# Kernel tuning notes

Hardware: AMD Instinct MI355X
Metric: run time of the kernel (lower is better)

The kernel has to match this reference:

```python
import jax, jax.numpy as jnp
import numpy as np

VOCAB, EMBED, HIDDEN = 50000, 256, 512
BATCH, SEQ = 64, 512


def setup_inputs() -> dict:
    key = jax.random.key(0)
    ks = jax.random.split(key, 20)
    s = 0.05  # small init scale to keep gates out of saturation
    inp = {
        "tokens": jax.random.randint(ks[0], (BATCH, SEQ), 0, VOCAB, dtype=jnp.int64),
        "emb": jax.random.normal(ks[1], (VOCAB, EMBED), jnp.float32) * s,
        "W1f": jax.random.normal(ks[2], (EMBED, 4 * HIDDEN), jnp.float32) * s,
        "U1f": jax.random.normal(ks[3], (HIDDEN, 4 * HIDDEN), jnp.float32) * s,
        "b1f": jax.random.normal(ks[4], (4 * HIDDEN,), jnp.float32) * s,
        "W2f": jax.random.normal(ks[5], (HIDDEN, 4 * HIDDEN), jnp.float32) * s,
        "U2f": jax.random.normal(ks[6], (HIDDEN, 4 * HIDDEN), jnp.float32) * s,
        "b2f": jax.random.normal(ks[7], (4 * HIDDEN,), jnp.float32) * s,
        "W1b": jax.random.normal(ks[8], (EMBED, 4 * HIDDEN), jnp.float32) * s,
        "U1b": jax.random.normal(ks[9], (HIDDEN, 4 * HIDDEN), jnp.float32) * s,
        "b1b": jax.random.normal(ks[10], (4 * HIDDEN,), jnp.float32) * s,
        "W2b": jax.random.normal(ks[11], (HIDDEN, 4 * HIDDEN), jnp.float32) * s,
        "U2b": jax.random.normal(ks[12], (HIDDEN, 4 * HIDDEN), jnp.float32) * s,
        "b2b": jax.random.normal(ks[13], (4 * HIDDEN,), jnp.float32) * s,
        "Wd": jax.random.normal(ks[14], (2 * HIDDEN, 5), jnp.float32) * s,
        "bd": jax.random.normal(ks[15], (5,), jnp.float32) * s,
    }
    return inp


def _lstm_cell(x, h, c, W, U, b):
    # Keras gate order: i, f, g (candidate), o
    z = x @ W + h @ U + b
    i, f, g, o = jnp.split(z, 4, axis=-1)
    c = jax.nn.sigmoid(f) * c + jax.nn.sigmoid(i) * jnp.tanh(g)
    h = jax.nn.sigmoid(o) * jnp.tanh(c)
    return h, c


def _run_stack(xs, W1, U1, b1, W2, U2, b2):
    # xs: [T, B, E]; stacked 2-layer LSTM, return last hidden of layer 2: [B, H]
    B = xs.shape[1]
    H = U1.shape[0]
    init = tuple(jnp.zeros((B, H), xs.dtype) for _ in range(4))

    def step(carry, x_t):
        h1, c1, h2, c2 = carry
        h1, c1 = _lstm_cell(x_t, h1, c1, W1, U1, b1)
        h2, c2 = _lstm_cell(h1, h2, c2, W2, U2, b2)
        return (h1, c1, h2, c2), None

    (h1, c1, h2, c2), _ = jax.lax.scan(step, init, xs)
    return h2


def reference(tokens, emb, W1f, U1f, b1f, W2f, U2f, b2f,
              W1b, U1b, b1b, W2b, U2b, b2b, Wd, bd):
    x = emb[tokens]                 # [B, T, E]
    xs = jnp.swapaxes(x, 0, 1)      # [T, B, E]
    h_fwd = _run_stack(xs, W1f, U1f, b1f, W2f, U2f, b2f)          # [B, H]
    h_bwd = _run_stack(xs[::-1], W1b, U1b, b1b, W2b, U2b, b2b)    # [B, H]
    feat = jnp.concatenate([h_fwd, h_bwd], axis=-1)               # [B, 2H]
    return feat @ Wd + bd                                         # [B, 5]
```

## Files before the change

### kernel.cpp

```cpp
#include <hip/hip_runtime.h>
#include <hip/hip_bf16.h>

#define TSEQ 512
#define NB   64
#define NE   256
#define NH   512
#define NG   2048

static const size_t OFF_W1  = 0;
static const size_t OFF_W2  = 6291456;
static const size_t OFF_X   = 14680064;
static const size_t OFF_H1  = 31457280;
static const size_t OFF_H2  = 31981568;
static const size_t OFF_HF  = 32505856;
static const size_t OFF_CNT = 32636928;

typedef __bf16 v8bf __attribute__((ext_vector_type(8)));
typedef float  v4f  __attribute__((ext_vector_type(4)));

#define MFMA16(a_, b_, c_) __builtin_amdgcn_mfma_f32_16x16x32_bf16((a_), (b_), (c_), 0, 0, 0)

static __device__ __forceinline__ v8bf load_h8(const __bf16* p) {
    unsigned long long lo = __hip_atomic_load((unsigned long long*)p,     __ATOMIC_RELAXED, __HIP_MEMORY_SCOPE_AGENT);
    unsigned long long hi = __hip_atomic_load((unsigned long long*)p + 1, __ATOMIC_RELAXED, __HIP_MEMORY_SCOPE_AGENT);
    union { unsigned long long q[2]; v8bf v; } u;
    u.q[0] = lo; u.q[1] = hi;
    return u.v;
}

static __device__ __forceinline__ unsigned short bf16_bits(float f) {
    __bf16 b = (__bf16)f;
    return __builtin_bit_cast(unsigned short, b);
}

__global__ void wconv_kernel(const float* __restrict__ Wf, const float* __restrict__ Uf,
                             const float* __restrict__ Wb, const float* __restrict__ Ub,
                             char* __restrict__ dst, int NC, int KX)
{
    int id = blockIdx.x * 256 + threadIdx.x;
    int j    = id & 7;
    int lane = (id >> 3) & 63;
    int t    = (id >> 9) & 1;
    int rest = id >> 10;
    int c    = rest % NC;
    int ds   = rest / NC;
    int slice = ds & 63;
    int dirr  = ds >> 6;
    int coll = t * 16 + (lane & 15);
    int k    = c * 32 + (lane >> 4) * 8 + j;
    int gate = coll >> 3, jjj = coll & 7;
    int zcol = gate * 512 + slice * 8 + jjj;
    const float* W = dirr ? Wb : Wf;
    const float* U = dirr ? Ub : Uf;
    float v = (k < KX) ? W[(size_t)k * NG + zcol] : U[(size_t)(k - KX) * NG + zcol];
    ((__bf16*)dst)[id] = (__bf16)v;
}

__global__ void gather_x_kernel(const int* __restrict__ tokens, const float* __restrict__ emb,
                                char* __restrict__ ws)
{
    size_t id = (size_t)blockIdx.x * 256 + threadIdx.x;
    int j  = (int)(id & 7);
    int m  = (int)((id >> 3) & 63);
    int kb = (int)((id >> 9) & 31);
    int t  = (int)(id >> 14);
    int tok = tokens[m * TSEQ + t];
    float v = emb[(size_t)tok * NE + kb * 8 + j];
    ((__bf16*)(ws + OFF_X))[(size_t)t * 16384 + (kb * 64 + m) * 8 + j] = (__bf16)v;
    if (id < 16384) ((int*)(ws + OFF_CNT))[id] = 0;
}

template<int LAYER>
__device__ void run_layer(char* __restrict__ ws, const char* __restrict__ smem,
                          int dir, int slice, int tid,
                          const float* __restrict__ bb)
{
    const int lane = tid & 63;
    const int wv   = tid >> 6;
    const int colc = lane & 15;
    const int q    = lane >> 4;
    const int m0   = wv * 16;
    const int jj   = colc & 7;
    const int hcol = slice * 8 + jj;

    __bf16* h1ring = (__bf16*)(ws + OFF_H1 + (size_t)dir * (4 * 65536));
    __bf16* h2ring = (__bf16*)(ws + OFF_H2 + (size_t)dir * (4 * 65536));
    const char* Xfrag = ws + OFF_X;
    __bf16* hfin = (__bf16*)(ws + OFF_HF) + (size_t)dir * (NB * NH);

    int* T = (int*)(ws + OFF_CNT);
    const int rep = ((slice << 2) | wv) & 15;
    int* p1   = T + (dir * 2 + 0) * 4096 + rep * 256 + wv * 64 + lane;
    int* p2   = T + (dir * 2 + 1) * 4096 + rep * 256 + wv * 64 + lane;
    int* ownb = T + (dir * 2 + LAYER) * 4096;

    const float bi  = bb[hcol];
    const float bf_ = bb[512 + hcol];
    const float bg  = bb[1024 + hcol];
    const float bo  = bb[1536 + hcol];

    float cst[4] = {0.f, 0.f, 0.f, 0.f};

    const int aoff = (m0 + colc) * 8;

    #pragma unroll 1
    for (int s = 0; s < TSEQ; ++s) {
        v4f acc0a = {0,0,0,0}, acc1a = {0,0,0,0};
        v4f acc0b = {0,0,0,0}, acc1b = {0,0,0,0};

        if (LAYER == 0) {
            const int xs = dir ? (TSEQ - 1 - s) : s;
            const char* xb = Xfrag + (size_t)xs * 32768;
            #pragma unroll
            for (int c = 0; c < 8; ++c) {
                v8bf a  = *(const v8bf*)(xb + (((4 * c + q) * 64 + m0 + colc) * 16));
                v8bf w0 = *(const v8bf*)(smem + (c * 2 + 0) * 1024 + lane * 16);
                v8bf w1 = *(const v8bf*)(smem + (c * 2 + 1) * 1024 + lane * 16);
                if (c & 1) { acc0b = MFMA16(a, w0, acc0b); acc1b = MFMA16(a, w1, acc1b); }
                else       { acc0a = MFMA16(a, w0, acc0a); acc1a = MFMA16(a, w1, acc1a); }
            }
        }

        {
            const int t1 = LAYER ? s + 1 : s;
            const int t2 = LAYER ? s : s - 3;
            if (t1 > 0) {
                while (true) {
                    int v1 = __hip_atomic_load(p1, __ATOMIC_RELAXED, __HIP_MEMORY_SCOPE_AGENT);
                    bool ok = (v1 >= t1);
                    if (t2 > 0) {
                        int v2 = __hip_atomic_load(p2, __ATOMIC_RELAXED, __HIP_MEMORY_SCOPE_AGENT);
                        ok = ok && (v2 >= t2);
                    }
                    if (__all(ok)) break;
                }
            }
        }

        if (LAYER == 0) {
            if (s > 0) {
                const __bf16* hb = h1ring + (size_t)((s - 1) & 3) * 32768;
                v8bf ah[16];
                #pragma unroll
                for (int c = 0; c < 16; ++c)
                    ah[c] = load_h8(hb + (4 * c + q) * 512 + aoff);
                __builtin_amdgcn_sched_barrier(0);
                #pragma unroll
                for (int c = 0; c < 16; ++c) {
                    v8bf w0 = *(const v8bf*)(smem + ((8 + c) * 2 + 0) * 1024 + lane * 16);
                    v8bf w1 = *(const v8bf*)(smem + ((8 + c) * 2 + 1) * 1024 + lane * 16);
                    if (c & 1) { acc0b = MFMA16(ah[c], w0, acc0b); acc1b = MFMA16(ah[c], w1, acc1b); }
                    else       { acc0a = MFMA16(ah[c], w0, acc0a); acc1a = MFMA16(ah[c], w1, acc1a); }
                }
            }
        } else {
            const __bf16* hb1 = h1ring + (size_t)(s & 3) * 32768;
            v8bf a0[16], a1[16];
            #pragma unroll
            for (int c = 0; c < 16; ++c)
                a0[c] = load_h8(hb1 + (4 * c + q) * 512 + aoff);
            if (s > 0) {
                const __bf16* hb2 = h2ring + (size_t)((s - 1) & 3) * 32768;
                #pragma unroll
                for (int c = 0; c < 16; ++c)
                    a1[c] = load_h8(hb2 + (4 * c + q) * 512 + aoff);
            }
            __builtin_amdgcn_sched_barrier(0);
            #pragma unroll
            for (int c = 0; c < 16; ++c) {
                v8bf w0 = *(const v8bf*)(smem + (c * 2 + 0) * 1024 + lane * 16);
                v8bf w1 = *(const v8bf*)(smem + (c * 2 + 1) * 1024 + lane * 16);
                if (c & 1) { acc0b = MFMA16(a0[c], w0, acc0b); acc1b = MFMA16(a0[c], w1, acc1b); }
                else       { acc0a = MFMA16(a0[c], w0, acc0a); acc1a = MFMA16(a0[c], w1, acc1a); }
            }
            if (s > 0) {
                #pragma unroll
                for (int c = 0; c < 16; ++c) {
                    v8bf w0 = *(const v8bf*)(smem + ((16 + c) * 2 + 0) * 1024 + lane * 16);
                    v8bf w1 = *(const v8bf*)(smem + ((16 + c) * 2 + 1) * 1024 + lane * 16);
                    if (c & 1) { acc0b = MFMA16(a1[c], w0, acc0b); acc1b = MFMA16(a1[c], w1, acc1b); }
                    else       { acc0a = MFMA16(a1[c], w0, acc0a); acc1a = MFMA16(a1[c], w1, acc1a); }
                }
            }
        }

        v4f z0 = acc0a + acc0b;
        v4f z1 = acc1a + acc1b;

        float hv[4];
        #pragma unroll
        for (int r = 0; r < 4; ++r) {
            float p0 = __shfl_xor(z0[r], 8, 64);
            float p1 = __shfl_xor(z1[r], 8, 64);
            float zi, zf, zg, zo;
            if (colc < 8) { zi = z0[r]; zf = p0;    zg = z1[r]; zo = p1;    }
            else          { zi = p0;    zf = z0[r]; zg = p1;    zo = z1[r]; }
            zi += bi; zf += bf_; zg += bg; zo += bo;
            float gi = 1.f / (1.f + __expf(-zi));
            float gf = 1.f / (1.f + __expf(-zf));
            float gg = 1.f - 2.f / (1.f + __expf(2.f * zg));
            float go = 1.f / (1.f + __expf(-zo));
            float cn = gf * cst[r] + gi * gg;
            cst[r] = cn;
            float th = 1.f - 2.f / (1.f + __expf(2.f * cn));
            hv[r] = go * th;
        }

        __bf16* hd = (LAYER ? h2ring : h1ring) + (size_t)(s & 3) * 32768;
        #pragma unroll
        for (int r = 0; r < 4; ++r) {
            float pv = __shfl_xor(hv[r], 1, 64);
            int m = m0 + q * 4 + r;
            if (((colc & 1) == 0) && (colc < 8)) {
                unsigned val = (unsigned)bf16_bits(hv[r]) | ((unsigned)bf16_bits(pv) << 16);
                __hip_atomic_store((unsigned*)(hd + (slice * 64 + m) * 8 + colc), val,
                                   __ATOMIC_RELAXED, __HIP_MEMORY_SCOPE_AGENT);
            }
            if (LAYER == 1 && s == TSEQ - 1 && colc < 8)
                hfin[(size_t)m * NH + hcol] = (__bf16)hv[r];
        }

        asm volatile("s_waitcnt vmcnt(0)" ::: "memory");
        if (lane < 16)
            __hip_atomic_store(ownb + lane * 256 + wv * 64 + slice, s + 1,
                               __ATOMIC_RELAXED, __HIP_MEMORY_SCOPE_AGENT);
    }
}

__global__ __launch_bounds__(256, 1) void lstm_persist(
    char* __restrict__ ws,
    const float* __restrict__ b1f, const float* __restrict__ b2f,
    const float* __restrict__ b1b, const float* __restrict__ b2b)
{
    const int tid   = threadIdx.x;
    const int bid   = blockIdx.x;
    const int dir   = bid >> 7;
    const int layer = (bid >> 6) & 1;
    const int slice = bid & 63;

    const int NC = layer ? 32 : 24;
    const int wbytes = NC * 2048;

    __shared__ char smem[65536];
    {
        const char* wsrc = ws + (layer ? OFF_W2 : OFF_W1)
                         + (size_t)(dir * 64 + slice) * (size_t)wbytes;
        for (int i = tid * 16; i < wbytes; i += 256 * 16)
            *(uint4*)(smem + i) = *(const uint4*)(wsrc + i);
    }
    __syncthreads();

    const float* bb = layer ? (dir ? b2b : b2f) : (dir ? b1b : b1f);
    if (layer == 0) run_layer<0>(ws, smem, dir, slice, tid, bb);
    else            run_layer<1>(ws, smem, dir, slice, tid, bb);
}

__global__ void head_kernel(const char* __restrict__ ws, const float* __restrict__ Wd,
                            const float* __restrict__ bd, float* __restrict__ out)
{
    int b = blockIdx.x;
    int lane = threadIdx.x;
    const __bf16* hfF = (const __bf16*)(ws + OFF_HF) + (size_t)b * NH;
    const __bf16* hfB = (const __bf16*)(ws + OFF_HF) + (size_t)(NB * NH) + (size_t)b * NH;
    #pragma unroll
    for (int o = 0; o < 5; ++o) {
        float sum = 0.f;
        for (int k = lane; k < 2 * NH; k += 64) {
            float fv = (k < NH) ? (float)hfF[k] : (float)hfB[k - NH];
            sum += fv * Wd[(size_t)k * 5 + o];
        }
        #pragma unroll
        for (int off = 32; off > 0; off >>= 1) sum += __shfl_down(sum, off, 64);
        if (lane == 0) out[b * 5 + o] = sum + bd[o];
    }
}

extern "C" void kernel_launch(void* const* d_in, const int* in_sizes, int n_in,
                              void* d_out, int out_size, void* d_ws, size_t ws_size,
                              hipStream_t stream)
{
    const int*   tokens = (const int*)  d_in[0];
    const float* emb    = (const float*)d_in[1];
    const float* W1f    = (const float*)d_in[2];
    const float* U1f    = (const float*)d_in[3];
    const float* b1f    = (const float*)d_in[4];
    const float* W2f    = (const float*)d_in[5];
    const float* U2f    = (const float*)d_in[6];
    const float* b2f    = (const float*)d_in[7];
    const float* W1b    = (const float*)d_in[8];
    const float* U1b    = (const float*)d_in[9];
    const float* b1b    = (const float*)d_in[10];
    const float* W2b    = (const float*)d_in[11];
    const float* U2b    = (const float*)d_in[12];
    const float* b2b    = (const float*)d_in[13];
    const float* Wd     = (const float*)d_in[14];
    const float* bd     = (const float*)d_in[15];
    char* ws = (char*)d_ws;

    wconv_kernel<<<12288, 256, 0, stream>>>(W1f, U1f, W1b, U1b, ws + OFF_W1, 24, 256);
    wconv_kernel<<<16384, 256, 0, stream>>>(W2f, U2f, W2b, U2b, ws + OFF_W2, 32, 512);
    gather_x_kernel<<<32768, 256, 0, stream>>>(tokens, emb, ws);
    lstm_persist<<<256, 256, 0, stream>>>(ws, b1f, b2f, b1b, b2b);
    head_kernel<<<NB, 64, 0, stream>>>(ws, Wd, bd, (float*)d_out);
}
```

Before: 3.545 ms.

## Validate hidden-state fragments with XOR shadow copies instead of draining stores

Each hidden-state write now also writes an XOR-masked shadow copy, with the mask alternating per ring pass. Readers reload until data and shadow agree, so the s_waitcnt vmcnt(0) before publishing the step counter can be removed. The ring shrinks from 4 to 3 slots, and layer 1 now waits on its two dependencies separately so it can start the h1 matmul before h2 is ready. The cost is doubled store and load traffic, possible retry loops, and reliance on relaxed-ordering assumptions for correctness.

```diff
diff --git a/kernel.cpp b/kernel.cpp
--- a/kernel.cpp
+++ b/kernel.cpp
@@ -11,9 +11,13 @@
 static const size_t OFF_W2  = 6291456;
 static const size_t OFF_X   = 14680064;
 static const size_t OFF_H1  = 31457280;
-static const size_t OFF_H2  = 31981568;
-static const size_t OFF_HF  = 32505856;
-static const size_t OFF_CNT = 32636928;
+static const size_t OFF_H2  = 31850496;
+static const size_t OFF_S1  = 32243712;
+static const size_t OFF_S2  = 32636928;
+static const size_t OFF_HF  = 33030144;
+static const size_t OFF_CNT = 33161216;
+
+#define SHDELTA 393216
 
 typedef __bf16 v8bf __attribute__((ext_vector_type(8)));
 typedef float  v4f  __attribute__((ext_vector_type(4)));
@@ -32,6 +36,34 @@
     __bf16 b = (__bf16)f;
     return __builtin_bit_cast(unsigned short, b);
 }
+
+static __device__ __forceinline__ unsigned frag_ok(v8bf d, v8bf sh, unsigned m) {
+    union { v8bf v; unsigned u[4]; } a, b;
+    a.v = d; b.v = sh;
+    unsigned x = (a.u[0] ^ b.u[0] ^ m) | (a.u[1] ^ b.u[1] ^ m)
+               | (a.u[2] ^ b.u[2] ^ m) | (a.u[3] ^ b.u[3] ^ m);
+    return (unsigned)(x == 0u);
+}
+
+#define LOAD_VALIDATE16(dst_, base_, mm_)                                      \
+    {                                                                          \
+        const __bf16* _b  = (base_);                                           \
+        const __bf16* _sb = _b + SHDELTA;                                      \
+        const unsigned _m = (mm_);                                             \
+        while (true) {                                                         \
+            v8bf _sh[16];                                                      \
+            _Pragma("unroll")                                                  \
+            for (int c = 0; c < 16; ++c) {                                     \
+                dst_[c] = load_h8(_b  + (4 * c + q) * 512 + aoff);             \
+                _sh[c]  = load_h8(_sb + (4 * c + q) * 512 + aoff);             \
+            }                                                                  \
+            __builtin_amdgcn_sched_barrier(0);                                 \
+            unsigned _ok = 1u;                                                 \
+            _Pragma("unroll")                                                  \
+            for (int c = 0; c < 16; ++c) _ok &= frag_ok(dst_[c], _sh[c], _m);  \
+            if (__all((int)_ok)) break;                                        \
+        }                                                                      \
+    }
 
 __global__ void wconv_kernel(const float* __restrict__ Wf, const float* __restrict__ Uf,
                              const float* __restrict__ Wb, const float* __restrict__ Ub,
@@ -67,6 +99,9 @@
     int tok = tokens[m * TSEQ + t];
     float v = emb[(size_t)tok * NE + kb * 8 + j];
     ((__bf16*)(ws + OFF_X))[(size_t)t * 16384 + (kb * 64 + m) * 8 + j] = (__bf16)v;
+    if (id < 393216) {
+        ((unsigned*)(ws + OFF_H1))[id] = (id < 196608) ? 0u : 0x3F803F80u;
+    }
     if (id < 16384) ((int*)(ws + OFF_CNT))[id] = 0;
 }
 
@@ -83,8 +118,8 @@
     const int jj   = colc & 7;
     const int hcol = slice * 8 + jj;
 
-    __bf16* h1ring = (__bf16*)(ws + OFF_H1 + (size_t)dir * (4 * 65536));
-    __bf16* h2ring = (__bf16*)(ws + OFF_H2 + (size_t)dir * (4 * 65536));
+    __bf16* h1ring = (__bf16*)(ws + OFF_H1 + (size_t)dir * (3 * 65536));
+    __bf16* h2ring = (__bf16*)(ws + OFF_H2 + (size_t)dir * (3 * 65536));
     const char* Xfrag = ws + OFF_X;
     __bf16* hfin = (__bf16*)(ws + OFF_HF) + (size_t)dir * (NB * NH);
 
@@ -103,48 +138,44 @@
 
     const int aoff = (m0 + colc) * 8;
 
+    int cs = 0, ps = 0, cp = 0, pp = 0;
+
     #pragma unroll 1
     for (int s = 0; s < TSEQ; ++s) {
         v4f acc0a = {0,0,0,0}, acc1a = {0,0,0,0};
         v4f acc0b = {0,0,0,0}, acc1b = {0,0,0,0};
 
         if (LAYER == 0) {
-            const int xs = dir ? (TSEQ - 1 - s) : s;
-            const char* xb = Xfrag + (size_t)xs * 32768;
-            #pragma unroll
-            for (int c = 0; c < 8; ++c) {
-                v8bf a  = *(const v8bf*)(xb + (((4 * c + q) * 64 + m0 + colc) * 16));
-                v8bf w0 = *(const v8bf*)(smem + (c * 2 + 0) * 1024 + lane * 16);
-                v8bf w1 = *(const v8bf*)(smem + (c * 2 + 1) * 1024 + lane * 16);
-                if (c & 1) { acc0b = MFMA16(a, w0, acc0b); acc1b = MFMA16(a, w1, acc1b); }
-                else       { acc0a = MFMA16(a, w0, acc0a); acc1a = MFMA16(a, w1, acc1a); }
-            }
-        }
-
-        {
-            const int t1 = LAYER ? s + 1 : s;
-            const int t2 = LAYER ? s : s - 3;
-            if (t1 > 0) {
-                while (true) {
-                    int v1 = __hip_atomic_load(p1, __ATOMIC_RELAXED, __HIP_MEMORY_SCOPE_AGENT);
-                    bool ok = (v1 >= t1);
-                    if (t2 > 0) {
-                        int v2 = __hip_atomic_load(p2, __ATOMIC_RELAXED, __HIP_MEMORY_SCOPE_AGENT);
-                        ok = ok && (v2 >= t2);
+            {
+                const int xs = dir ? (TSEQ - 1 - s) : s;
+                const char* xb = Xfrag + (size_t)xs * 32768;
+                #pragma unroll
+                for (int c = 0; c < 8; ++c) {
+                    v8bf a  = *(const v8bf*)(xb + (((4 * c + q) * 64 + m0 + colc) * 16));
+                    v8bf w0 = *(const v8bf*)(smem + (c * 2 + 0) * 1024 + lane * 16);
+                    v8bf w1 = *(const v8bf*)(smem + (c * 2 + 1) * 1024 + lane * 16);
+                    if (c & 1) { acc0b = MFMA16(a, w0, acc0b); acc1b = MFMA16(a, w1, acc1b); }
+                    else       { acc0a = MFMA16(a, w0, acc0a); acc1a = MFMA16(a, w1, acc1a); }
+                }
+            }
+            {
+                const int t1 = s;
+                const int t2 = s - 2;
+                if (t1 > 0) {
+                    while (true) {
+                        int v1 = __hip_atomic_load(p1, __ATOMIC_RELAXED, __HIP_MEMORY_SCOPE_AGENT);
+                        bool ok = (v1 >= t1);
+                        if (t2 > 0) {
+                            int v2 = __hip_atomic_load(p2, __ATOMIC_RELAXED, __HIP_MEMORY_SCOPE_AGENT);
+                            ok = ok && (v2 >= t2);
+                        }
+                        if (__all(ok)) break;
                     }
-                    if (__all(ok)) break;
-                }
-            }
-        }
-
-        if (LAYER == 0) {
+                }
+            }
             if (s > 0) {
-                const __bf16* hb = h1ring + (size_t)((s - 1) & 3) * 32768;
                 v8bf ah[16];
-                #pragma unroll
-                for (int c = 0; c < 16; ++c)
-                    ah[c] = load_h8(hb + (4 * c + q) * 512 + aoff);
-                __builtin_amdgcn_sched_barrier(0);
+                LOAD_VALIDATE16(ah, h1ring + (size_t)ps * 32768, pp ? 0x40004000u : 0u);
                 #pragma unroll
                 for (int c = 0; c < 16; ++c) {
                     v8bf w0 = *(const v8bf*)(smem + ((8 + c) * 2 + 0) * 1024 + lane * 16);
@@ -154,26 +185,31 @@
                 }
             }
         } else {
-            const __bf16* hb1 = h1ring + (size_t)(s & 3) * 32768;
-            v8bf a0[16], a1[16];
-            #pragma unroll
-            for (int c = 0; c < 16; ++c)
-                a0[c] = load_h8(hb1 + (4 * c + q) * 512 + aoff);
+            {
+                const int t1 = s + 1;
+                while (true) {
+                    int v1 = __hip_atomic_load(p1, __ATOMIC_RELAXED, __HIP_MEMORY_SCOPE_AGENT);
+                    if (__all(v1 >= t1)) break;
+                }
+            }
+            {
+                v8bf a0[16];
+                LOAD_VALIDATE16(a0, h1ring + (size_t)cs * 32768, cp ? 0x40004000u : 0u);
+                #pragma unroll
+                for (int c = 0; c < 16; ++c) {
+                    v8bf w0 = *(const v8bf*)(smem + (c * 2 + 0) * 1024 + lane * 16);
+                    v8bf w1 = *(const v8bf*)(smem + (c * 2 + 1) * 1024 + lane * 16);
+                    if (c & 1) { acc0b = MFMA16(a0[c], w0, acc0b); acc1b = MFMA16(a0[c], w1, acc1b); }
+                    else       { acc0a = MFMA16(a0[c], w0, acc0a); acc1a = MFMA16(a0[c], w1, acc1a); }
+                }
+            }
             if (s > 0) {
-                const __bf16* hb2 = h2ring + (size_t)((s - 1) & 3) * 32768;
-                #pragma unroll
-                for (int c = 0; c < 16; ++c)
-                    a1[c] = load_h8(hb2 + (4 * c + q) * 512 + aoff);
-            }
-            __builtin_amdgcn_sched_barrier(0);
-            #pragma unroll
-            for (int c = 0; c < 16; ++c) {
-                v8bf w0 = *(const v8bf*)(smem + (c * 2 + 0) * 1024 + lane * 16);
-                v8bf w1 = *(const v8bf*)(smem + (c * 2 + 1) * 1024 + lane * 16);
-                if (c & 1) { acc0b = MFMA16(a0[c], w0, acc0b); acc1b = MFMA16(a0[c], w1, acc1b); }
-                else       { acc0a = MFMA16(a0[c], w0, acc0a); acc1a = MFMA16(a0[c], w1, acc1a); }
-            }
-            if (s > 0) {
+                while (true) {
+                    int v2 = __hip_atomic_load(p2, __ATOMIC_RELAXED, __HIP_MEMORY_SCOPE_AGENT);
+                    if (__all(v2 >= s)) break;
+                }
+                v8bf a1[16];
+                LOAD_VALIDATE16(a1, h2ring + (size_t)ps * 32768, pp ? 0x40004000u : 0u);
                 #pragma unroll
                 for (int c = 0; c < 16; ++c) {
                     v8bf w0 = *(const v8bf*)(smem + ((16 + c) * 2 + 0) * 1024 + lane * 16);
@@ -191,10 +227,10 @@
         #pragma unroll
         for (int r = 0; r < 4; ++r) {
             float p0 = __shfl_xor(z0[r], 8, 64);
-            float p1 = __shfl_xor(z1[r], 8, 64);
+            float p1v = __shfl_xor(z1[r], 8, 64);
             float zi, zf, zg, zo;
-            if (colc < 8) { zi = z0[r]; zf = p0;    zg = z1[r]; zo = p1;    }
-            else          { zi = p0;    zf = z0[r]; zg = p1;    zo = z1[r]; }
+            if (colc < 8) { zi = z0[r]; zf = p0;    zg = z1[r]; zo = p1v;   }
+            else          { zi = p0;    zf = z0[r]; zg = p1v;   zo = z1[r]; }
             zi += bi; zf += bf_; zg += bg; zo += bo;
             float gi = 1.f / (1.f + __expf(-zi));
             float gf = 1.f / (1.f + __expf(-zf));
@@ -206,7 +242,8 @@
             hv[r] = go * th;
         }
 
-        __bf16* hd = (LAYER ? h2ring : h1ring) + (size_t)(s & 3) * 32768;
+        __bf16* hd = (LAYER ? h2ring : h1ring) + (size_t)cs * 32768;
+        const unsigned mw = cp ? 0x40004000u : 0u;
         #pragma unroll
         for (int r = 0; r < 4; ++r) {
             float pv = __shfl_xor(hv[r], 1, 64);
@@ -215,15 +252,21 @@
                 unsigned val = (unsigned)bf16_bits(hv[r]) | ((unsigned)bf16_bits(pv) << 16);
                 __hip_atomic_store((unsigned*)(hd + (slice * 64 + m) * 8 + colc), val,
                                    __ATOMIC_RELAXED, __HIP_MEMORY_SCOPE_AGENT);
+                __hip_atomic_store((unsigned*)(hd + SHDELTA + (slice * 64 + m) * 8 + colc), val ^ mw,
+                                   __ATOMIC_RELAXED, __HIP_MEMORY_SCOPE_AGENT);
             }
             if (LAYER == 1 && s == TSEQ - 1 && colc < 8)
                 hfin[(size_t)m * NH + hcol] = (__bf16)hv[r];
         }
 
-        asm volatile("s_waitcnt vmcnt(0)" ::: "memory");
+        __builtin_amdgcn_sched_barrier(0);
         if (lane < 16)
             __hip_atomic_store(ownb + lane * 256 + wv * 64 + slice, s + 1,
                                __ATOMIC_RELAXED, __HIP_MEMORY_SCOPE_AGENT);
+
+        ps = cs; pp = cp;
+        cs = (cs == 2) ? 0 : cs + 1;
+        if (cs == 0) cp ^= 1;
     }
 }
 
```

Result: slower. 4.779 ms (+34.8%).

## Embed parity tag bits in hidden-state payload to validate ring reads without store fence

Applied to the files above, without the earlier changes.

Hidden values are clamped to below 1 so bit 14 of each bf16 is free, and that bit now carries a per-ring-lap parity tag. Readers check the tag on every loaded fragment and spin until all fragments match, then clear the bit. This lets writers drop the s_waitcnt vmcnt(0) before publishing their step counter. The risk is that counters can become visible before the data, which the tag check is meant to catch, and the clamp slightly changes numerics.

```diff
diff --git a/kernel.cpp b/kernel.cpp
--- a/kernel.cpp
+++ b/kernel.cpp
@@ -32,6 +32,53 @@
     __bf16 b = (__bf16)f;
     return __builtin_bit_cast(unsigned short, b);
 }
+
+static __device__ __forceinline__ unsigned frag_chk_clr(v8bf* f, unsigned pm) {
+    union { v8bf v; unsigned u[4]; } a; a.v = *f;
+    unsigned bad = ((a.u[0] ^ pm) | (a.u[1] ^ pm) | (a.u[2] ^ pm) | (a.u[3] ^ pm)) & 0x40004000u;
+    a.u[0] &= 0xBFFFBFFFu; a.u[1] &= 0xBFFFBFFFu;
+    a.u[2] &= 0xBFFFBFFFu; a.u[3] &= 0xBFFFBFFFu;
+    *f = a.v;
+    return bad;
+}
+
+#define LOAD_VALIDATE16(dst_, base_, pm_)                                      \
+    {                                                                          \
+        const __bf16* _b  = (base_);                                           \
+        const unsigned _pm = (pm_);                                            \
+        while (true) {                                                         \
+            _Pragma("unroll")                                                  \
+            for (int c = 0; c < 16; ++c)                                       \
+                dst_[c] = load_h8(_b + (4 * c + q) * 512 + aoff);              \
+            __builtin_amdgcn_sched_barrier(0);                                 \
+            unsigned _bad = 0u;                                                \
+            _Pragma("unroll")                                                  \
+            for (int c = 0; c < 16; ++c) _bad |= frag_chk_clr(&dst_[c], _pm);  \
+            if (__all(_bad == 0u)) break;                                      \
+        }                                                                      \
+    }
+
+#define LOAD_VALIDATE32(d0_, b0_, pm0_, d1_, b1_, pm1_)                        \
+    {                                                                          \
+        const __bf16* _b0 = (b0_);                                             \
+        const __bf16* _b1 = (b1_);                                             \
+        const unsigned _p0 = (pm0_), _p1 = (pm1_);                             \
+        while (true) {                                                         \
+            _Pragma("unroll")                                                  \
+            for (int c = 0; c < 16; ++c)                                       \
+                d0_[c] = load_h8(_b0 + (4 * c + q) * 512 + aoff);              \
+            _Pragma("unroll")                                                  \
+            for (int c = 0; c < 16; ++c)                                       \
+                d1_[c] = load_h8(_b1 + (4 * c + q) * 512 + aoff);              \
+            __builtin_amdgcn_sched_barrier(0);                                 \
+            unsigned _bad = 0u;                                                \
+            _Pragma("unroll")                                                  \
+            for (int c = 0; c < 16; ++c) _bad |= frag_chk_clr(&d0_[c], _p0);   \
+            _Pragma("unroll")                                                  \
+            for (int c = 0; c < 16; ++c) _bad |= frag_chk_clr(&d1_[c], _p1);   \
+            if (__all(_bad == 0u)) break;                                      \
+        }                                                                      \
+    }
 
 __global__ void wconv_kernel(const float* __restrict__ Wf, const float* __restrict__ Uf,
                              const float* __restrict__ Wb, const float* __restrict__ Ub,
@@ -67,7 +114,8 @@
     int tok = tokens[m * TSEQ + t];
     float v = emb[(size_t)tok * NE + kb * 8 + j];
     ((__bf16*)(ws + OFF_X))[(size_t)t * 16384 + (kb * 64 + m) * 8 + j] = (__bf16)v;
-    if (id < 16384) ((int*)(ws + OFF_CNT))[id] = 0;
+    if (id < 262144) ((unsigned*)(ws + OFF_H1))[id] = 0x40004000u;
+    if (id < 16384)  ((int*)(ws + OFF_CNT))[id] = 0;
 }
 
 template<int LAYER>
@@ -107,6 +155,9 @@
     for (int s = 0; s < TSEQ; ++s) {
         v4f acc0a = {0,0,0,0}, acc1a = {0,0,0,0};
         v4f acc0b = {0,0,0,0}, acc1b = {0,0,0,0};
+
+        const unsigned pmW  = ((s >> 2) & 1)       ? 0x40004000u : 0u;
+        const unsigned pmRp = (((s - 1) >> 2) & 1) ? 0x40004000u : 0u;
 
         if (LAYER == 0) {
             const int xs = dir ? (TSEQ - 1 - s) : s;
@@ -139,12 +190,8 @@
 
         if (LAYER == 0) {
             if (s > 0) {
-                const __bf16* hb = h1ring + (size_t)((s - 1) & 3) * 32768;
                 v8bf ah[16];
-                #pragma unroll
-                for (int c = 0; c < 16; ++c)
-                    ah[c] = load_h8(hb + (4 * c + q) * 512 + aoff);
-                __builtin_amdgcn_sched_barrier(0);
+                LOAD_VALIDATE16(ah, h1ring + (size_t)((s - 1) & 3) * 32768, pmRp);
                 #pragma unroll
                 for (int c = 0; c < 16; ++c) {
                     v8bf w0 = *(const v8bf*)(smem + ((8 + c) * 2 + 0) * 1024 + lane * 16);
@@ -154,18 +201,14 @@
                 }
             }
         } else {
-            const __bf16* hb1 = h1ring + (size_t)(s & 3) * 32768;
+            const unsigned pmRc = pmW;
             v8bf a0[16], a1[16];
-            #pragma unroll
-            for (int c = 0; c < 16; ++c)
-                a0[c] = load_h8(hb1 + (4 * c + q) * 512 + aoff);
             if (s > 0) {
-                const __bf16* hb2 = h2ring + (size_t)((s - 1) & 3) * 32768;
-                #pragma unroll
-                for (int c = 0; c < 16; ++c)
-                    a1[c] = load_h8(hb2 + (4 * c + q) * 512 + aoff);
-            }
-            __builtin_amdgcn_sched_barrier(0);
+                LOAD_VALIDATE32(a0, h1ring + (size_t)(s & 3) * 32768, pmRc,
+                                a1, h2ring + (size_t)((s - 1) & 3) * 32768, pmRp);
+            } else {
+                LOAD_VALIDATE16(a0, h1ring + (size_t)(s & 3) * 32768, pmRc);
+            }
             #pragma unroll
             for (int c = 0; c < 16; ++c) {
                 v8bf w0 = *(const v8bf*)(smem + (c * 2 + 0) * 1024 + lane * 16);
@@ -191,10 +234,10 @@
         #pragma unroll
         for (int r = 0; r < 4; ++r) {
             float p0 = __shfl_xor(z0[r], 8, 64);
-            float p1 = __shfl_xor(z1[r], 8, 64);
+            float p1v = __shfl_xor(z1[r], 8, 64);
             float zi, zf, zg, zo;
-            if (colc < 8) { zi = z0[r]; zf = p0;    zg = z1[r]; zo = p1;    }
-            else          { zi = p0;    zf = z0[r]; zg = p1;    zo = z1[r]; }
+            if (colc < 8) { zi = z0[r]; zf = p0;    zg = z1[r]; zo = p1v;   }
+            else          { zi = p0;    zf = z0[r]; zg = p1v;   zo = z1[r]; }
             zi += bi; zf += bf_; zg += bg; zo += bo;
             float gi = 1.f / (1.f + __expf(-zi));
             float gf = 1.f / (1.f + __expf(-zf));
@@ -203,7 +246,7 @@
             float cn = gf * cst[r] + gi * gg;
             cst[r] = cn;
             float th = 1.f - 2.f / (1.f + __expf(2.f * cn));
-            hv[r] = go * th;
+            hv[r] = fminf(fmaxf(go * th, -0.99609375f), 0.99609375f);
         }
 
         __bf16* hd = (LAYER ? h2ring : h1ring) + (size_t)(s & 3) * 32768;
@@ -212,7 +255,7 @@
             float pv = __shfl_xor(hv[r], 1, 64);
             int m = m0 + q * 4 + r;
             if (((colc & 1) == 0) && (colc < 8)) {
-                unsigned val = (unsigned)bf16_bits(hv[r]) | ((unsigned)bf16_bits(pv) << 16);
+                unsigned val = ((unsigned)bf16_bits(hv[r]) | ((unsigned)bf16_bits(pv) << 16)) | pmW;
                 __hip_atomic_store((unsigned*)(hd + (slice * 64 + m) * 8 + colc), val,
                                    __ATOMIC_RELAXED, __HIP_MEMORY_SCOPE_AGENT);
             }
@@ -220,7 +263,7 @@
                 hfin[(size_t)m * NH + hcol] = (__bf16)hv[r];
         }
 
-        asm volatile("s_waitcnt vmcnt(0)" ::: "memory");
+        __builtin_amdgcn_sched_barrier(0);
         if (lane < 16)
             __hip_atomic_store(ownb + lane * 256 + wv * 64 + slice, s + 1,
                                __ATOMIC_RELAXED, __HIP_MEMORY_SCOPE_AGENT);
```

New measurement: 3.675 ms. 1.04x slower.

## Halve persistent LSTM grid so each block owns two hidden slices

Applied to the files above, without the earlier changes.

The persistent LSTM kernel now launches 128 blocks instead of 256, and each block processes two adjacent 8-column hidden slices. It loads both weight tiles into up to 128 KB of dynamic shared memory and reuses each activation fragment across twice as many MFMAs. It also adds a short s_sleep in the spin-wait loop to reduce polling pressure. The aim is fewer participants in the per-step cross-block synchronization and better reuse of the loaded h fragments. The cost is twice the serial MFMA and gate work per block on the critical recurrent path, and the sleep can add wake-up latency.

```diff
diff --git a/kernel.cpp b/kernel.cpp
--- a/kernel.cpp
+++ b/kernel.cpp
@@ -72,7 +72,7 @@
 
 template<int LAYER>
 __device__ void run_layer(char* __restrict__ ws, const char* __restrict__ smem,
-                          int dir, int slice, int tid,
+                          int dir, int jp, int tid,
                           const float* __restrict__ bb)
 {
     const int lane = tid & 63;
@@ -81,7 +81,9 @@
     const int q    = lane >> 4;
     const int m0   = wv * 16;
     const int jj   = colc & 7;
-    const int hcol = slice * 8 + jj;
+    const int sA   = jp * 2;
+    const int sB   = sA + 1;
+    const int WB   = LAYER ? 65536 : 49152;
 
     __bf16* h1ring = (__bf16*)(ws + OFF_H1 + (size_t)dir * (4 * 65536));
     __bf16* h2ring = (__bf16*)(ws + OFF_H2 + (size_t)dir * (4 * 65536));
@@ -89,35 +91,49 @@
     __bf16* hfin = (__bf16*)(ws + OFF_HF) + (size_t)dir * (NB * NH);
 
     int* T = (int*)(ws + OFF_CNT);
-    const int rep = ((slice << 2) | wv) & 15;
+    const int rep = ((sA << 2) | wv) & 15;
     int* p1   = T + (dir * 2 + 0) * 4096 + rep * 256 + wv * 64 + lane;
     int* p2   = T + (dir * 2 + 1) * 4096 + rep * 256 + wv * 64 + lane;
     int* ownb = T + (dir * 2 + LAYER) * 4096;
 
-    const float bi  = bb[hcol];
-    const float bf_ = bb[512 + hcol];
-    const float bg  = bb[1024 + hcol];
-    const float bo  = bb[1536 + hcol];
-
-    float cst[4] = {0.f, 0.f, 0.f, 0.f};
+    float bi[2], bf_[2], bg_[2], bo_[2];
+    #pragma unroll
+    for (int g = 0; g < 2; ++g) {
+        const int hc = (sA + g) * 8 + jj;
+        bi[g]  = bb[hc];
+        bf_[g] = bb[512 + hc];
+        bg_[g] = bb[1024 + hc];
+        bo_[g] = bb[1536 + hc];
+    }
+
+    float cst[2][4] = {{0.f,0.f,0.f,0.f},{0.f,0.f,0.f,0.f}};
 
     const int aoff = (m0 + colc) * 8;
 
     #pragma unroll 1
     for (int s = 0; s < TSEQ; ++s) {
-        v4f acc0a = {0,0,0,0}, acc1a = {0,0,0,0};
-        v4f acc0b = {0,0,0,0}, acc1b = {0,0,0,0};
+        v4f az[2][2][2];
+        #pragma unroll
+        for (int g = 0; g < 2; ++g)
+            #pragma unroll
+            for (int p = 0; p < 2; ++p)
+                #pragma unroll
+                for (int ab = 0; ab < 2; ++ab)
+                    az[g][p][ab] = (v4f){0.f, 0.f, 0.f, 0.f};
 
         if (LAYER == 0) {
             const int xs = dir ? (TSEQ - 1 - s) : s;
             const char* xb = Xfrag + (size_t)xs * 32768;
             #pragma unroll
             for (int c = 0; c < 8; ++c) {
-                v8bf a  = *(const v8bf*)(xb + (((4 * c + q) * 64 + m0 + colc) * 16));
-                v8bf w0 = *(const v8bf*)(smem + (c * 2 + 0) * 1024 + lane * 16);
-                v8bf w1 = *(const v8bf*)(smem + (c * 2 + 1) * 1024 + lane * 16);
-                if (c & 1) { acc0b = MFMA16(a, w0, acc0b); acc1b = MFMA16(a, w1, acc1b); }
-                else       { acc0a = MFMA16(a, w0, acc0a); acc1a = MFMA16(a, w1, acc1a); }
+                v8bf a = *(const v8bf*)(xb + (((4 * c + q) * 64 + m0 + colc) * 16));
+                #pragma unroll
+                for (int g = 0; g < 2; ++g) {
+                    v8bf w0 = *(const v8bf*)(smem + g * WB + (c * 2 + 0) * 1024 + lane * 16);
+                    v8bf w1 = *(const v8bf*)(smem + g * WB + (c * 2 + 1) * 1024 + lane * 16);
+                    az[g][0][c & 1] = MFMA16(a, w0, az[g][0][c & 1]);
+                    az[g][1][c & 1] = MFMA16(a, w1, az[g][1][c & 1]);
+                }
             }
         }
 
@@ -133,6 +149,7 @@
                         ok = ok && (v2 >= t2);
                     }
                     if (__all(ok)) break;
+                    __builtin_amdgcn_s_sleep(4);
                 }
             }
         }
@@ -147,10 +164,13 @@
                 __builtin_amdgcn_sched_barrier(0);
                 #pragma unroll
                 for (int c = 0; c < 16; ++c) {
-                    v8bf w0 = *(const v8bf*)(smem + ((8 + c) * 2 + 0) * 1024 + lane * 16);
-                    v8bf w1 = *(const v8bf*)(smem + ((8 + c) * 2 + 1) * 1024 + lane * 16);
-                    if (c & 1) { acc0b = MFMA16(ah[c], w0, acc0b); acc1b = MFMA16(ah[c], w1, acc1b); }
-                    else       { acc0a = MFMA16(ah[c], w0, acc0a); acc1a = MFMA16(ah[c], w1, acc1a); }
+                    #pragma unroll
+                    for (int g = 0; g < 2; ++g) {
+                        v8bf w0 = *(const v8bf*)(smem + g * WB + ((8 + c) * 2 + 0) * 1024 + lane * 16);
+                        v8bf w1 = *(const v8bf*)(smem + g * WB + ((8 + c) * 2 + 1) * 1024 + lane * 16);
+                        az[g][0][c & 1] = MFMA16(ah[c], w0, az[g][0][c & 1]);
+                        az[g][1][c & 1] = MFMA16(ah[c], w1, az[g][1][c & 1]);
+                    }
                 }
             }
         } else {
@@ -168,62 +188,77 @@
             __builtin_amdgcn_sched_barrier(0);
             #pragma unroll
             for (int c = 0; c < 16; ++c) {
-                v8bf w0 = *(const v8bf*)(smem + (c * 2 + 0) * 1024 + lane * 16);
-                v8bf w1 = *(const v8bf*)(smem + (c * 2 + 1) * 1024 + lane * 16);
-                if (c & 1) { acc0b = MFMA16(a0[c], w0, acc0b); acc1b = MFMA16(a0[c], w1, acc1b); }
-                else       { acc0a = MFMA16(a0[c], w0, acc0a); acc1a = MFMA16(a0[c], w1, acc1a); }
+                #pragma unroll
+                for (int g = 0; g < 2; ++g) {
+                    v8bf w0 = *(const v8bf*)(smem + g * WB + (c * 2 + 0) * 1024 + lane * 16);
+                    v8bf w1 = *(const v8bf*)(smem + g * WB + (c * 2 + 1) * 1024 + lane * 16);
+                    az[g][0][c & 1] = MFMA16(a0[c], w0, az[g][0][c & 1]);
+                    az[g][1][c & 1] = MFMA16(a0[c], w1, az[g][1][c & 1]);
+                }
             }
             if (s > 0) {
                 #pragma unroll
                 for (int c = 0; c < 16; ++c) {
-                    v8bf w0 = *(const v8bf*)(smem + ((16 + c) * 2 + 0) * 1024 + lane * 16);
-                    v8bf w1 = *(const v8bf*)(smem + ((16 + c) * 2 + 1) * 1024 + lane * 16);
-                    if (c & 1) { acc0b = MFMA16(a1[c], w0, acc0b); acc1b = MFMA16(a1[c], w1, acc1b); }
-                    else       { acc0a = MFMA16(a1[c], w0, acc0a); acc1a = MFMA16(a1[c], w1, acc1a); }
-                }
-            }
-        }
-
-        v4f z0 = acc0a + acc0b;
-        v4f z1 = acc1a + acc1b;
-
-        float hv[4];
+                    #pragma unroll
+                    for (int g = 0; g < 2; ++g) {
+                        v8bf w0 = *(const v8bf*)(smem + g * WB + ((16 + c) * 2 + 0) * 1024 + lane * 16);
+                        v8bf w1 = *(const v8bf*)(smem + g * WB + ((16 + c) * 2 + 1) * 1024 + lane * 16);
+                        az[g][0][c & 1] = MFMA16(a1[c], w0, az[g][0][c & 1]);
+                        az[g][1][c & 1] = MFMA16(a1[c], w1, az[g][1][c & 1]);
+                    }
+                }
+            }
+        }
+
+        float hv[2][4];
         #pragma unroll
-        for (int r = 0; r < 4; ++r) {
-            float p0 = __shfl_xor(z0[r], 8, 64);
-            float p1 = __shfl_xor(z1[r], 8, 64);
-            float zi, zf, zg, zo;
-            if (colc < 8) { zi = z0[r]; zf = p0;    zg = z1[r]; zo = p1;    }
-            else          { zi = p0;    zf = z0[r]; zg = p1;    zo = z1[r]; }
-            zi += bi; zf += bf_; zg += bg; zo += bo;
-            float gi = 1.f / (1.f + __expf(-zi));
-            float gf = 1.f / (1.f + __expf(-zf));
-            float gg = 1.f - 2.f / (1.f + __expf(2.f * zg));
-            float go = 1.f / (1.f + __expf(-zo));
-            float cn = gf * cst[r] + gi * gg;
-            cst[r] = cn;
-            float th = 1.f - 2.f / (1.f + __expf(2.f * cn));
-            hv[r] = go * th;
+        for (int g = 0; g < 2; ++g) {
+            v4f z0 = az[g][0][0] + az[g][0][1];
+            v4f z1 = az[g][1][0] + az[g][1][1];
+            #pragma unroll
+            for (int r = 0; r < 4; ++r) {
+                float p0 = __shfl_xor(z0[r], 8, 64);
+                float p1v = __shfl_xor(z1[r], 8, 64);
+                float zi, zf, zg, zo;
+                if (colc < 8) { zi = z0[r]; zf = p0;    zg = z1[r]; zo = p1v;   }
+                else          { zi = p0;    zf = z0[r]; zg = p1v;   zo = z1[r]; }
+                zi += bi[g]; zf += bf_[g]; zg += bg_[g]; zo += bo_[g];
+                float gi = 1.f / (1.f + __expf(-zi));
+                float gf = 1.f / (1.f + __expf(-zf));
+                float gg = 1.f - 2.f / (1.f + __expf(2.f * zg));
+                float go = 1.f / (1.f + __expf(-zo));
+                float cn = gf * cst[g][r] + gi * gg;
+                cst[g][r] = cn;
+                float th = 1.f - 2.f / (1.f + __expf(2.f * cn));
+                hv[g][r] = go * th;
+            }
         }
 
         __bf16* hd = (LAYER ? h2ring : h1ring) + (size_t)(s & 3) * 32768;
         #pragma unroll
-        for (int r = 0; r < 4; ++r) {
-            float pv = __shfl_xor(hv[r], 1, 64);
-            int m = m0 + q * 4 + r;
-            if (((colc & 1) == 0) && (colc < 8)) {
-                unsigned val = (unsigned)bf16_bits(hv[r]) | ((unsigned)bf16_bits(pv) << 16);
-                __hip_atomic_store((unsigned*)(hd + (slice * 64 + m) * 8 + colc), val,
-                                   __ATOMIC_RELAXED, __HIP_MEMORY_SCOPE_AGENT);
-            }
-            if (LAYER == 1 && s == TSEQ - 1 && colc < 8)
-                hfin[(size_t)m * NH + hcol] = (__bf16)hv[r];
+        for (int g = 0; g < 2; ++g) {
+            const int sl = sA + g;
+            #pragma unroll
+            for (int r = 0; r < 4; ++r) {
+                float pv = __shfl_xor(hv[g][r], 1, 64);
+                int m = m0 + q * 4 + r;
+                if (((colc & 1) == 0) && (colc < 8)) {
+                    unsigned val = (unsigned)bf16_bits(hv[g][r]) | ((unsigned)bf16_bits(pv) << 16);
+                    __hip_atomic_store((unsigned*)(hd + (sl * 64 + m) * 8 + colc), val,
+                                       __ATOMIC_RELAXED, __HIP_MEMORY_SCOPE_AGENT);
+                }
+                if (LAYER == 1 && s == TSEQ - 1 && colc < 8)
+                    hfin[(size_t)m * NH + sl * 8 + jj] = (__bf16)hv[g][r];
+            }
         }
 
         asm volatile("s_waitcnt vmcnt(0)" ::: "memory");
-        if (lane < 16)
-            __hip_atomic_store(ownb + lane * 256 + wv * 64 + slice, s + 1,
+        if (lane < 16) {
+            __hip_atomic_store(ownb + lane * 256 + wv * 64 + sA, s + 1,
                                __ATOMIC_RELAXED, __HIP_MEMORY_SCOPE_AGENT);
+            __hip_atomic_store(ownb + lane * 256 + wv * 64 + sB, s + 1,
+                               __ATOMIC_RELAXED, __HIP_MEMORY_SCOPE_AGENT);
+        }
     }
 }
 
@@ -232,27 +267,26 @@
     const float* __restrict__ b1f, const float* __restrict__ b2f,
     const float* __restrict__ b1b, const float* __restrict__ b2b)
 {
+    extern __shared__ char smem[];
     const int tid   = threadIdx.x;
     const int bid   = blockIdx.x;
-    const int dir   = bid >> 7;
-    const int layer = (bid >> 6) & 1;
-    const int slice = bid & 63;
-
-    const int NC = layer ? 32 : 24;
-    const int wbytes = NC * 2048;
-
-    __shared__ char smem[65536];
+    const int dir   = bid >> 6;
+    const int layer = (bid >> 5) & 1;
+    const int jp    = bid & 31;
+
+    const int WB = layer ? 65536 : 49152;
     {
         const char* wsrc = ws + (layer ? OFF_W2 : OFF_W1)
-                         + (size_t)(dir * 64 + slice) * (size_t)wbytes;
-        for (int i = tid * 16; i < wbytes; i += 256 * 16)
+                         + (size_t)(dir * 64 + jp * 2) * (size_t)WB;
+        const int total = 2 * WB;
+        for (int i = tid * 16; i < total; i += 256 * 16)
             *(uint4*)(smem + i) = *(const uint4*)(wsrc + i);
     }
     __syncthreads();
 
     const float* bb = layer ? (dir ? b2b : b2f) : (dir ? b1b : b1f);
-    if (layer == 0) run_layer<0>(ws, smem, dir, slice, tid, bb);
-    else            run_layer<1>(ws, smem, dir, slice, tid, bb);
+    if (layer == 0) run_layer<0>(ws, smem, dir, jp, tid, bb);
+    else            run_layer<1>(ws, smem, dir, jp, tid, bb);
 }
 
 __global__ void head_kernel(const char* __restrict__ ws, const float* __restrict__ Wd,
@@ -297,9 +331,16 @@
     const float* bd     = (const float*)d_in[15];
     char* ws = (char*)d_ws;
 
+    static int attr_set = 0;
+    if (!attr_set) {
+        hipFuncSetAttribute(reinterpret_cast<const void*>(lstm_persist),
+                            hipFuncAttributeMaxDynamicSharedMemorySize, 131072);
+        attr_set = 1;
+    }
+
     wconv_kernel<<<12288, 256, 0, stream>>>(W1f, U1f, W1b, U1b, ws + OFF_W1, 24, 256);
     wconv_kernel<<<16384, 256, 0, stream>>>(W2f, U2f, W2b, U2b, ws + OFF_W2, 32, 512);
     gather_x_kernel<<<32768, 256, 0, stream>>>(tokens, emb, ws);
-    lstm_persist<<<256, 256, 0, stream>>>(ws, b1f, b2f, b1b, b2b);
+    lstm_persist<<<128, 256, 131072, stream>>>(ws, b1f, b2f, b1b, b2b);
     head_kernel<<<NB, 64, 0, stream>>>(ws, Wd, bd, (float*)d_out);
 }
```

After: 3.958 ms. 1.12x slower.
